# Kernel tuning notes

Hardware: AMD Instinct MI355X
Metric: run time of the kernel (lower is better)

The kernel has to match this reference:

```python
import jax, jax.numpy as jnp
import numpy as np

N, H, W, K = 4, 512, 512, 8
V, F = 50000, 100000
SIGMA, GAMMA = 1e-4, 1e-4
ZNEAR, ZFAR = 1.0, 100.0
EPS = 1e-10


def setup_inputs() -> dict:
    key = jax.random.key(0)
    k1, k2, k3, k4, k5, k6 = jax.random.split(key, 6)
    vn = jax.random.normal(k1, (V, 3), dtype=jnp.float32)
    verts_normals = vn / jnp.linalg.norm(vn, axis=-1, keepdims=True)
    bary = jax.random.uniform(k2, (N, H, W, K, 3), dtype=jnp.float32)
    bary_coords = bary / bary.sum(-1, keepdims=True)  # valid barycentrics
    dists = jax.random.normal(k3, (N, H, W, K), dtype=jnp.float32) * 1e-4
    zbuf = jax.random.uniform(k4, (N, H, W, K), dtype=jnp.float32) * (ZFAR - ZNEAR) + ZNEAR
    faces = jax.random.randint(k5, (F, 3), 0, V, dtype=jnp.int64)
    # include -1 entries (background pixels), as in real rasterizer output
    pix_to_face = jax.random.randint(k6, (N, H, W, K), -1, F, dtype=jnp.int64)
    return {"verts_normals": verts_normals, "bary_coords": bary_coords,
            "dists": dists, "zbuf": zbuf, "faces": faces,
            "pix_to_face": pix_to_face}


def reference(verts_normals, bary_coords, dists, zbuf, faces, pix_to_face):
    # --- normal_shading: gather + barycentric interpolation of vertex normals ---
    faces_normals = verts_normals[faces]                      # (F, 3verts, 3)
    mask = pix_to_face >= 0                                   # (N,H,W,K)
    idx = jnp.where(mask, pix_to_face, 0)
    attrs = faces_normals[idx]                                # (N,H,W,K,3verts,3)
    colors = jnp.einsum('nhwkv,nhwkvc->nhwkc', bary_coords, attrs)
    colors = colors * mask[..., None]                         # zero masked pixels
    opacity = jnp.ones(mask.shape, dtype=colors.dtype)        # torch.ones_like
    # --- softmax_rgb_blend ---
    maskf = mask.astype(colors.dtype)
    prob_map = jax.nn.sigmoid(-dists / SIGMA) * maskf
    alpha = jnp.prod(1.0 - prob_map, axis=-1)                 # (N,H,W)
    z_inv = (ZFAR - zbuf) / (ZFAR - ZNEAR) * maskf
    z_inv_max = jnp.max(z_inv, axis=-1, keepdims=True)
    weights_num = prob_map * jnp.exp((z_inv - z_inv_max) / GAMMA) * opacity
    delta = jnp.maximum(jnp.exp((EPS - z_inv_max) / GAMMA), EPS)
    denom = weights_num.sum(-1, keepdims=True) + delta        # (N,H,W,1)
    background = jnp.array([1.0, 1.0, 1.0], dtype=colors.dtype)
    weighted_colors = jnp.einsum('nhwk,nhwkc->nhwc', weights_num, colors)
    rgb = (weighted_colors + delta * background) / denom      # (N,H,W,3)
    a = (1.0 - alpha)[..., None]                              # (N,H,W,1)
    return jnp.concatenate([rgb, a], axis=-1)                 # (N,H,W,4)
```

## Files before the change

### kernel.cpp

```cpp
#include <hip/hip_runtime.h>
#include <hip/hip_fp16.h>


constexpr int   N_PIX      = 4 * 512 * 512;
constexpr int   N_FRAG     = N_PIX * 8;
constexpr int   N_BLOCKS   = 2048;
constexpr int   N_THREADS  = N_BLOCKS * 256;
constexpr int   N_ITERS    = N_FRAG / N_THREADS;
constexpr float INV_SIGMA  = 1.0f / 1e-4f;
constexpr float INV_GAMMA  = 1.0f / 1e-4f;
constexpr float ZFARV      = 100.0f;
constexpr float INV_ZRANGE = 1.0f / 99.0f;
constexpr float EPSV       = 1e-10f;

__global__ __launch_bounds__(256)
void build_face_normals_kernel(const float* __restrict__ vn,
                               const int*   __restrict__ faces,
                               __half*      __restrict__ fnh,
                               int nf)
{
    int f = blockIdx.x * blockDim.x + threadIdx.x;
    if (f >= nf) return;
    int v0 = faces[3 * f + 0];
    int v1 = faces[3 * f + 1];
    int v2 = faces[3 * f + 2];
    union { ushort us[16]; uint4 u4[2]; } row;
    row.us[0] = __half_as_ushort(__float2half(vn[3 * v0 + 0]));
    row.us[1] = __half_as_ushort(__float2half(vn[3 * v0 + 1]));
    row.us[2] = __half_as_ushort(__float2half(vn[3 * v0 + 2]));
    row.us[3] = __half_as_ushort(__float2half(vn[3 * v1 + 0]));
    row.us[4] = __half_as_ushort(__float2half(vn[3 * v1 + 1]));
    row.us[5] = __half_as_ushort(__float2half(vn[3 * v1 + 2]));
    row.us[6] = __half_as_ushort(__float2half(vn[3 * v2 + 0]));
    row.us[7] = __half_as_ushort(__float2half(vn[3 * v2 + 1]));
    row.us[8] = __half_as_ushort(__float2half(vn[3 * v2 + 2]));
    row.us[9] = 0; row.us[10] = 0; row.us[11] = 0;
    row.us[12] = 0; row.us[13] = 0; row.us[14] = 0; row.us[15] = 0;
    uint4* dst = reinterpret_cast<uint4*>(fnh + 16 * (size_t)f);
    dst[0] = row.u4[0];
    dst[1] = row.u4[1];
}

__global__ __launch_bounds__(256, 8)
void shade_kernel(const float*  __restrict__ bary,
                  const float*  __restrict__ dists,
                  const float*  __restrict__ zbuf,
                  const int*    __restrict__ p2f,
                  const __half* __restrict__ fnh,
                  float*        __restrict__ out)
{
    int gid = blockIdx.x * 256 + threadIdx.x;
    int kk  = threadIdx.x & 7;

    float nd  = dists[gid];
    float nz  = zbuf[gid];
    int   nf_ = p2f[gid];
    size_t nbo = 3 * (size_t)gid;
    float nb0 = bary[nbo + 0];
    float nb1 = bary[nbo + 1];
    float nb2 = bary[nbo + 2];

#pragma unroll
    for (int it = 0; it < N_ITERS; ++it) {
        float d  = nd, zb = nz;
        int   f  = nf_;
        float b0 = nb0, b1 = nb1, b2 = nb2;

        int gn = gid + N_THREADS;
        if (it + 1 < N_ITERS) {
            nd  = dists[gn];
            nz  = zbuf[gn];
            nf_ = p2f[gn];
            size_t bo = 3 * (size_t)gn;
            nb0 = bary[bo + 0];
            nb1 = bary[bo + 1];
            nb2 = bary[bo + 2];
        }

        bool  m  = f >= 0;
        float pr = m ? __builtin_amdgcn_rcpf(1.0f + __expf(d * INV_SIGMA)) : 0.0f;
        float zi = m ? (ZFARV - zb) * INV_ZRANGE : 0.0f;

        float zmax = zi;
        zmax = fmaxf(zmax, __shfl_xor(zmax, 1));
        zmax = fmaxf(zmax, __shfl_xor(zmax, 2));
        zmax = fmaxf(zmax, __shfl_xor(zmax, 4));

        float am = 1.0f - pr;
        am *= __shfl_xor(am, 1);
        am *= __shfl_xor(am, 2);
        am *= __shfl_xor(am, 4);

        float w  = pr * __expf((zi - zmax) * INV_GAMMA);
        int   fe = (w != 0.0f) ? f : 0;

        const __half* hp = fnh + 16 * (size_t)fe;
        uint4 a  = *reinterpret_cast<const uint4*>(hp);
        uint  b8 = reinterpret_cast<const uint*>(hp)[4];
        float2 q0 = __half22float2(*reinterpret_cast<const __half2*>(&a.x));
        float2 q1 = __half22float2(*reinterpret_cast<const __half2*>(&a.y));
        float2 q2 = __half22float2(*reinterpret_cast<const __half2*>(&a.z));
        float2 q3 = __half22float2(*reinterpret_cast<const __half2*>(&a.w));
        float2 q4 = __half22float2(*reinterpret_cast<const __half2*>(&b8));

        float cr = w * (b0 * q0.x + b1 * q1.y + b2 * q3.x);
        float cg = w * (b0 * q0.y + b1 * q2.x + b2 * q3.y);
        float cb = w * (b0 * q1.x + b1 * q2.y + b2 * q4.x);
        float ws = w;

        ws += __shfl_xor(ws, 1);  cr += __shfl_xor(cr, 1);
        cg += __shfl_xor(cg, 1);  cb += __shfl_xor(cb, 1);
        ws += __shfl_xor(ws, 2);  cr += __shfl_xor(cr, 2);
        cg += __shfl_xor(cg, 2);  cb += __shfl_xor(cb, 2);
        ws += __shfl_xor(ws, 4);  cr += __shfl_xor(cr, 4);
        cg += __shfl_xor(cg, 4);  cb += __shfl_xor(cb, 4);

        if (kk == 0) {
            float delta     = fmaxf(__expf((EPSV - zmax) * INV_GAMMA), EPSV);
            float inv_denom = __builtin_amdgcn_rcpf(ws + delta);
            float4 o;
            o.x = (cr + delta) * inv_denom;
            o.y = (cg + delta) * inv_denom;
            o.z = (cb + delta) * inv_denom;
            o.w = 1.0f - am;
            reinterpret_cast<float4*>(out)[gid >> 3] = o;
        }
        gid = gn;
    }
}

extern "C" void kernel_launch(void* const* d_in, const int* in_sizes, int n_in,
                              void* d_out, int out_size, void* d_ws, size_t ws_size,
                              hipStream_t stream) {
    const float* vn    = (const float*)d_in[0];
    const float* bary  = (const float*)d_in[1];
    const float* dists = (const float*)d_in[2];
    const float* zbuf  = (const float*)d_in[3];
    const int*   faces = (const int*)d_in[4];
    const int*   p2f   = (const int*)d_in[5];
    float*       out   = (float*)d_out;

    int nf = in_sizes[4] / 3;
    __half* fnh = (__half*)d_ws;

    build_face_normals_kernel<<<(nf + 255) / 256, 256, 0, stream>>>(vn, faces, fnh, nf);
    shade_kernel<<<N_BLOCKS, 256, 0, stream>>>(bary, dists, zbuf, p2f, fnh, out);
}
```

Before: 232.7 us.

## Split shading into weight pass and sparse gather-resolve pass over surviving fragments

The fused shading kernel becomes two passes. The first reads fragments with float4 vector loads, two threads per pixel, and computes the softmax weights. It compacts the at most two fragments with nonzero weight into a 32-byte per-pixel slot holding face ids and fp16-packed weighted barycentrics. The second pass gathers face normals only for those surviving faces, falling back to a full 8-fragment recompute when more survive. This targets the per-fragment random gathers in the face-normal table, at the cost of an extra kernel launch, a slot buffer write and read, and fp16 rounding of the weighted barycentrics.

```diff
diff --git a/kernel.cpp b/kernel.cpp
--- a/kernel.cpp
+++ b/kernel.cpp
@@ -4,14 +4,23 @@
 
 constexpr int   N_PIX      = 4 * 512 * 512;
 constexpr int   N_FRAG     = N_PIX * 8;
-constexpr int   N_BLOCKS   = 2048;
-constexpr int   N_THREADS  = N_BLOCKS * 256;
-constexpr int   N_ITERS    = N_FRAG / N_THREADS;
 constexpr float INV_SIGMA  = 1.0f / 1e-4f;
 constexpr float INV_GAMMA  = 1.0f / 1e-4f;
 constexpr float ZFARV      = 100.0f;
 constexpr float INV_ZRANGE = 1.0f / 99.0f;
 constexpr float EPSV       = 1e-10f;
+
+__device__ __forceinline__ uint pack_h2(float a, float b) {
+    uint ua = (uint)__half_as_ushort(__float2half_rn(a));
+    uint ub = (uint)__half_as_ushort(__float2half_rn(b));
+    return ua | (ub << 16);
+}
+__device__ __forceinline__ float unp_lo(uint u) {
+    return __half2float(__ushort_as_half((ushort)(u & 0xffffu)));
+}
+__device__ __forceinline__ float unp_hi(uint u) {
+    return __half2float(__ushort_as_half((ushort)(u >> 16)));
+}
 
 __global__ __launch_bounds__(256)
 void build_face_normals_kernel(const float* __restrict__ vn,
@@ -41,91 +50,276 @@
     dst[1] = row.u4[1];
 }
 
-__global__ __launch_bounds__(256, 8)
-void shade_kernel(const float*  __restrict__ bary,
-                  const float*  __restrict__ dists,
-                  const float*  __restrict__ zbuf,
-                  const int*    __restrict__ p2f,
-                  const __half* __restrict__ fnh,
-                  float*        __restrict__ out)
+__global__ __launch_bounds__(256)
+void p1_weights_kernel(const float4* __restrict__ bary4,
+                       const float4* __restrict__ d4p,
+                       const float4* __restrict__ z4p,
+                       const int4*   __restrict__ f4p,
+                       uint4*        __restrict__ slots)
 {
     int gid = blockIdx.x * 256 + threadIdx.x;
-    int kk  = threadIdx.x & 7;
-
-    float nd  = dists[gid];
-    float nz  = zbuf[gid];
-    int   nf_ = p2f[gid];
-    size_t nbo = 3 * (size_t)gid;
-    float nb0 = bary[nbo + 0];
-    float nb1 = bary[nbo + 1];
-    float nb2 = bary[nbo + 2];
-
-#pragma unroll
-    for (int it = 0; it < N_ITERS; ++it) {
-        float d  = nd, zb = nz;
-        int   f  = nf_;
-        float b0 = nb0, b1 = nb1, b2 = nb2;
-
-        int gn = gid + N_THREADS;
-        if (it + 1 < N_ITERS) {
-            nd  = dists[gn];
-            nz  = zbuf[gn];
-            nf_ = p2f[gn];
-            size_t bo = 3 * (size_t)gn;
-            nb0 = bary[bo + 0];
-            nb1 = bary[bo + 1];
-            nb2 = bary[bo + 2];
-        }
-
-        bool  m  = f >= 0;
-        float pr = m ? __builtin_amdgcn_rcpf(1.0f + __expf(d * INV_SIGMA)) : 0.0f;
-        float zi = m ? (ZFARV - zb) * INV_ZRANGE : 0.0f;
-
-        float zmax = zi;
-        zmax = fmaxf(zmax, __shfl_xor(zmax, 1));
-        zmax = fmaxf(zmax, __shfl_xor(zmax, 2));
-        zmax = fmaxf(zmax, __shfl_xor(zmax, 4));
-
-        float am = 1.0f - pr;
-        am *= __shfl_xor(am, 1);
-        am *= __shfl_xor(am, 2);
-        am *= __shfl_xor(am, 4);
-
-        float w  = pr * __expf((zi - zmax) * INV_GAMMA);
-        int   fe = (w != 0.0f) ? f : 0;
-
-        const __half* hp = fnh + 16 * (size_t)fe;
-        uint4 a  = *reinterpret_cast<const uint4*>(hp);
-        uint  b8 = reinterpret_cast<const uint*>(hp)[4];
-        float2 q0 = __half22float2(*reinterpret_cast<const __half2*>(&a.x));
-        float2 q1 = __half22float2(*reinterpret_cast<const __half2*>(&a.y));
-        float2 q2 = __half22float2(*reinterpret_cast<const __half2*>(&a.z));
-        float2 q3 = __half22float2(*reinterpret_cast<const __half2*>(&a.w));
-        float2 q4 = __half22float2(*reinterpret_cast<const __half2*>(&b8));
-
-        float cr = w * (b0 * q0.x + b1 * q1.y + b2 * q3.x);
-        float cg = w * (b0 * q0.y + b1 * q2.x + b2 * q3.y);
-        float cb = w * (b0 * q1.x + b1 * q2.y + b2 * q4.x);
-        float ws = w;
-
-        ws += __shfl_xor(ws, 1);  cr += __shfl_xor(cr, 1);
-        cg += __shfl_xor(cg, 1);  cb += __shfl_xor(cb, 1);
-        ws += __shfl_xor(ws, 2);  cr += __shfl_xor(cr, 2);
-        cg += __shfl_xor(cg, 2);  cb += __shfl_xor(cb, 2);
-        ws += __shfl_xor(ws, 4);  cr += __shfl_xor(cr, 4);
-        cg += __shfl_xor(cg, 4);  cb += __shfl_xor(cb, 4);
-
-        if (kk == 0) {
-            float delta     = fmaxf(__expf((EPSV - zmax) * INV_GAMMA), EPSV);
-            float inv_denom = __builtin_amdgcn_rcpf(ws + delta);
-            float4 o;
-            o.x = (cr + delta) * inv_denom;
-            o.y = (cg + delta) * inv_denom;
-            o.z = (cb + delta) * inv_denom;
-            o.w = 1.0f - am;
-            reinterpret_cast<float4*>(out)[gid >> 3] = o;
-        }
-        gid = gn;
+    int h   = gid & 1;
+
+    float4 d4 = d4p[gid];
+    float4 z4 = z4p[gid];
+    int4   f4 = f4p[gid];
+    const float4* bp = bary4 + 3 * (size_t)gid;
+    float4 b0 = bp[0], b1 = bp[1], b2 = bp[2];
+
+    float dk[4] = {d4.x, d4.y, d4.z, d4.w};
+    float zk[4] = {z4.x, z4.y, z4.z, z4.w};
+    int   fk[4] = {f4.x, f4.y, f4.z, f4.w};
+    float bf[12] = {b0.x, b0.y, b0.z, b0.w, b1.x, b1.y, b1.z, b1.w,
+                    b2.x, b2.y, b2.z, b2.w};
+
+    float pr[4], zi[4];
+#pragma unroll
+    for (int k = 0; k < 4; ++k) {
+        bool m = fk[k] >= 0;
+        pr[k] = m ? __builtin_amdgcn_rcpf(1.0f + __expf(dk[k] * INV_SIGMA)) : 0.0f;
+        zi[k] = m ? (ZFARV - zk[k]) * INV_ZRANGE : 0.0f;
+    }
+
+    float zmax = fmaxf(fmaxf(zi[0], zi[1]), fmaxf(zi[2], zi[3]));
+    zmax = fmaxf(zmax, __shfl_xor(zmax, 1));
+
+    float am = (1.0f - pr[0]) * (1.0f - pr[1]) * (1.0f - pr[2]) * (1.0f - pr[3]);
+    am *= __shfl_xor(am, 1);
+
+    float w[4];
+#pragma unroll
+    for (int k = 0; k < 4; ++k)
+        w[k] = pr[k] * __expf((zi[k] - zmax) * INV_GAMMA);
+
+    float ws = (w[0] + w[1]) + (w[2] + w[3]);
+    ws += __shfl_xor(ws, 1);
+
+    float delta = fmaxf(__expf((EPSV - zmax) * INV_GAMMA), EPSV);
+    float inv   = __builtin_amdgcn_rcpf(ws + delta);
+    float base  = delta * inv;
+
+    int   lf0 = -1, lf1 = -1, lcnt = 0;
+    float c0x = 0.f, c0y = 0.f, c0z = 0.f;
+    float c1x = 0.f, c1y = 0.f, c1z = 0.f;
+#pragma unroll
+    for (int k = 0; k < 4; ++k) {
+        if (w[k] != 0.0f) {
+            float cw = w[k] * inv;
+            if (lcnt == 0) {
+                lf0 = fk[k];
+                c0x = cw * bf[3 * k + 0];
+                c0y = cw * bf[3 * k + 1];
+                c0z = cw * bf[3 * k + 2];
+            } else if (lcnt == 1) {
+                lf1 = fk[k];
+                c1x = cw * bf[3 * k + 0];
+                c1y = cw * bf[3 * k + 1];
+                c1z = cw * bf[3 * k + 2];
+            }
+            ++lcnt;
+        }
+    }
+
+    int   pcnt = __shfl_xor(lcnt, 1);
+    int   pf0  = __shfl_xor(lf0, 1);
+    int   pf1  = __shfl_xor(lf1, 1);
+    float p0x = __shfl_xor(c0x, 1), p0y = __shfl_xor(c0y, 1), p0z = __shfl_xor(c0z, 1);
+    float p1x = __shfl_xor(c1x, 1), p1y = __shfl_xor(c1y, 1), p1z = __shfl_xor(c1z, 1);
+
+    int total = lcnt + pcnt;
+    int   F0, F1;
+    float S0x, S0y, S0z, S1x, S1y, S1z;
+    if (lcnt == 0) {
+        F0 = pf0; S0x = p0x; S0y = p0y; S0z = p0z;
+        F1 = pf1; S1x = p1x; S1y = p1y; S1z = p1z;
+    } else if (lcnt == 1) {
+        F0 = lf0; S0x = c0x; S0y = c0y; S0z = c0z;
+        F1 = pf0; S1x = p0x; S1y = p0y; S1z = p0z;
+    } else {
+        F0 = lf0; S0x = c0x; S0y = c0y; S0z = c0z;
+        F1 = lf1; S1x = c1x; S1y = c1y; S1z = c1z;
+    }
+    if (total > 2) F1 = -2;
+
+    if (h == 0) {
+        int pix = gid >> 1;
+        uint4 q0;
+        q0.x = __float_as_uint(base);
+        q0.y = __float_as_uint(am);
+        q0.z = (uint)F0;
+        q0.w = (uint)F1;
+        uint4 q1;
+        q1.x = pack_h2(S0x, S0y);
+        q1.y = pack_h2(S0z, S1x);
+        q1.z = pack_h2(S1y, S1z);
+        q1.w = 0u;
+        slots[2 * (size_t)pix + 0] = q0;
+        slots[2 * (size_t)pix + 1] = q1;
+    }
+}
+
+__global__ __launch_bounds__(256)
+void p2_resolve_kernel(const uint4*  __restrict__ slots,
+                       const __half* __restrict__ fnh,
+                       const float*  __restrict__ dists,
+                       const float*  __restrict__ zbuf,
+                       const int*    __restrict__ p2f,
+                       const float*  __restrict__ bary,
+                       float4*       __restrict__ out)
+{
+    int pix = blockIdx.x * 256 + threadIdx.x;
+    if (pix >= N_PIX) return;
+
+    uint4 q0 = slots[2 * (size_t)pix + 0];
+    uint4 q1 = slots[2 * (size_t)pix + 1];
+    float base = __uint_as_float(q0.x);
+    float am   = __uint_as_float(q0.y);
+    int   F0   = (int)q0.z;
+    int   F1   = (int)q0.w;
+
+    float r, g, b;
+
+    if (F1 != -2) {
+        r = base; g = base; b = base;
+        if (F0 >= 0) {
+            const __half* hp = fnh + 16 * (size_t)F0;
+            uint4 a  = *reinterpret_cast<const uint4*>(hp);
+            uint  b8 = reinterpret_cast<const uint*>(hp)[4];
+            float2 n01 = __half22float2(*reinterpret_cast<const __half2*>(&a.x));
+            float2 n23 = __half22float2(*reinterpret_cast<const __half2*>(&a.y));
+            float2 n45 = __half22float2(*reinterpret_cast<const __half2*>(&a.z));
+            float2 n67 = __half22float2(*reinterpret_cast<const __half2*>(&a.w));
+            float2 n8x = __half22float2(*reinterpret_cast<const __half2*>(&b8));
+            float cb0 = unp_lo(q1.x), cb1 = unp_hi(q1.x), cb2 = unp_lo(q1.y);
+            r += cb0 * n01.x + cb1 * n23.y + cb2 * n67.x;
+            g += cb0 * n01.y + cb1 * n45.x + cb2 * n67.y;
+            b += cb0 * n23.x + cb1 * n45.y + cb2 * n8x.x;
+        }
+        if (F1 >= 0) {
+            const __half* hp = fnh + 16 * (size_t)F1;
+            uint4 a  = *reinterpret_cast<const uint4*>(hp);
+            uint  b8 = reinterpret_cast<const uint*>(hp)[4];
+            float2 n01 = __half22float2(*reinterpret_cast<const __half2*>(&a.x));
+            float2 n23 = __half22float2(*reinterpret_cast<const __half2*>(&a.y));
+            float2 n45 = __half22float2(*reinterpret_cast<const __half2*>(&a.z));
+            float2 n67 = __half22float2(*reinterpret_cast<const __half2*>(&a.w));
+            float2 n8x = __half22float2(*reinterpret_cast<const __half2*>(&b8));
+            float cb0 = unp_hi(q1.y), cb1 = unp_lo(q1.z), cb2 = unp_hi(q1.z);
+            r += cb0 * n01.x + cb1 * n23.y + cb2 * n67.x;
+            g += cb0 * n01.y + cb1 * n45.x + cb2 * n67.y;
+            b += cb0 * n23.x + cb1 * n45.y + cb2 * n8x.x;
+        }
+    } else {
+        float pr8[8], zi8[8], w8[8];
+        int   ff8[8];
+        float zmax = 0.0f;
+        am = 1.0f;
+#pragma unroll
+        for (int k = 0; k < 8; ++k) {
+            float d  = dists[8 * (size_t)pix + k];
+            float zb = zbuf[8 * (size_t)pix + k];
+            int   f  = p2f[8 * (size_t)pix + k];
+            ff8[k] = f;
+            bool m = f >= 0;
+            pr8[k] = m ? __builtin_amdgcn_rcpf(1.0f + __expf(d * INV_SIGMA)) : 0.0f;
+            zi8[k] = m ? (ZFARV - zb) * INV_ZRANGE : 0.0f;
+            zmax   = fmaxf(zmax, zi8[k]);
+            am    *= (1.0f - pr8[k]);
+        }
+        float ws = 0.0f;
+#pragma unroll
+        for (int k = 0; k < 8; ++k) {
+            w8[k] = pr8[k] * __expf((zi8[k] - zmax) * INV_GAMMA);
+            ws += w8[k];
+        }
+        float delta = fmaxf(__expf((EPSV - zmax) * INV_GAMMA), EPSV);
+        float inv   = __builtin_amdgcn_rcpf(ws + delta);
+        base = delta * inv;
+        r = base; g = base; b = base;
+#pragma unroll
+        for (int k = 0; k < 8; ++k) {
+            if (w8[k] != 0.0f) {
+                float cw = w8[k] * inv;
+                float bb0 = bary[24 * (size_t)pix + 3 * k + 0];
+                float bb1 = bary[24 * (size_t)pix + 3 * k + 1];
+                float bb2 = bary[24 * (size_t)pix + 3 * k + 2];
+                const __half* hp = fnh + 16 * (size_t)ff8[k];
+                uint4 a  = *reinterpret_cast<const uint4*>(hp);
+                uint  b8v = reinterpret_cast<const uint*>(hp)[4];
+                float2 n01 = __half22float2(*reinterpret_cast<const __half2*>(&a.x));
+                float2 n23 = __half22float2(*reinterpret_cast<const __half2*>(&a.y));
+                float2 n45 = __half22float2(*reinterpret_cast<const __half2*>(&a.z));
+                float2 n67 = __half22float2(*reinterpret_cast<const __half2*>(&a.w));
+                float2 n8x = __half22float2(*reinterpret_cast<const __half2*>(&b8v));
+                r += cw * (bb0 * n01.x + bb1 * n23.y + bb2 * n67.x);
+                g += cw * (bb0 * n01.y + bb1 * n45.x + bb2 * n67.y);
+                b += cw * (bb0 * n23.x + bb1 * n45.y + bb2 * n8x.x);
+            }
+        }
+    }
+
+    float4 o;
+    o.x = r; o.y = g; o.z = b; o.w = 1.0f - am;
+    out[pix] = o;
+}
+
+__global__ __launch_bounds__(256)
+void shade_fallback_kernel(const float*  __restrict__ bary,
+                           const float*  __restrict__ dists,
+                           const float*  __restrict__ zbuf,
+                           const int*    __restrict__ p2f,
+                           const __half* __restrict__ fnh,
+                           float*        __restrict__ out)
+{
+    int gid = blockIdx.x * 256 + threadIdx.x;
+    if (gid >= N_FRAG) return;
+    int kk = gid & 7;
+    float d  = dists[gid];
+    float zb = zbuf[gid];
+    int   f  = p2f[gid];
+    float b0 = bary[3 * (size_t)gid + 0];
+    float b1 = bary[3 * (size_t)gid + 1];
+    float b2 = bary[3 * (size_t)gid + 2];
+    bool  m  = f >= 0;
+    float pr = m ? __builtin_amdgcn_rcpf(1.0f + __expf(d * INV_SIGMA)) : 0.0f;
+    float zi = m ? (ZFARV - zb) * INV_ZRANGE : 0.0f;
+    float zmax = zi;
+    zmax = fmaxf(zmax, __shfl_xor(zmax, 1));
+    zmax = fmaxf(zmax, __shfl_xor(zmax, 2));
+    zmax = fmaxf(zmax, __shfl_xor(zmax, 4));
+    float am = 1.0f - pr;
+    am *= __shfl_xor(am, 1);
+    am *= __shfl_xor(am, 2);
+    am *= __shfl_xor(am, 4);
+    float w  = pr * __expf((zi - zmax) * INV_GAMMA);
+    int   fe = (w != 0.0f) ? f : 0;
+    const __half* hp = fnh + 16 * (size_t)fe;
+    uint4 a  = *reinterpret_cast<const uint4*>(hp);
+    uint  b8 = reinterpret_cast<const uint*>(hp)[4];
+    float2 n01 = __half22float2(*reinterpret_cast<const __half2*>(&a.x));
+    float2 n23 = __half22float2(*reinterpret_cast<const __half2*>(&a.y));
+    float2 n45 = __half22float2(*reinterpret_cast<const __half2*>(&a.z));
+    float2 n67 = __half22float2(*reinterpret_cast<const __half2*>(&a.w));
+    float2 n8x = __half22float2(*reinterpret_cast<const __half2*>(&b8));
+    float cr = w * (b0 * n01.x + b1 * n23.y + b2 * n67.x);
+    float cg = w * (b0 * n01.y + b1 * n45.x + b2 * n67.y);
+    float cb = w * (b0 * n23.x + b1 * n45.y + b2 * n8x.x);
+    float ws = w;
+    ws += __shfl_xor(ws, 1);  cr += __shfl_xor(cr, 1);
+    cg += __shfl_xor(cg, 1);  cb += __shfl_xor(cb, 1);
+    ws += __shfl_xor(ws, 2);  cr += __shfl_xor(cr, 2);
+    cg += __shfl_xor(cg, 2);  cb += __shfl_xor(cb, 2);
+    ws += __shfl_xor(ws, 4);  cr += __shfl_xor(cr, 4);
+    cg += __shfl_xor(cg, 4);  cb += __shfl_xor(cb, 4);
+    if (kk == 0) {
+        float delta     = fmaxf(__expf((EPSV - zmax) * INV_GAMMA), EPSV);
+        float inv_denom = __builtin_amdgcn_rcpf(ws + delta);
+        float4 o;
+        o.x = (cr + delta) * inv_denom;
+        o.y = (cg + delta) * inv_denom;
+        o.z = (cb + delta) * inv_denom;
+        o.w = 1.0f - am;
+        reinterpret_cast<float4*>(out)[gid >> 3] = o;
     }
 }
 
@@ -141,8 +335,26 @@
     float*       out   = (float*)d_out;
 
     int nf = in_sizes[4] / 3;
+
+    size_t table_bytes = (size_t)nf * 32;
+    size_t slot_bytes  = (size_t)N_PIX * 32;
     __half* fnh = (__half*)d_ws;
 
     build_face_normals_kernel<<<(nf + 255) / 256, 256, 0, stream>>>(vn, faces, fnh, nf);
-    shade_kernel<<<N_BLOCKS, 256, 0, stream>>>(bary, dists, zbuf, p2f, fnh, out);
-}
+
+    if (ws_size >= table_bytes + slot_bytes) {
+        uint4* slots = (uint4*)((char*)d_ws + table_bytes);
+        p1_weights_kernel<<<(N_PIX * 2) / 256, 256, 0, stream>>>(
+            reinterpret_cast<const float4*>(bary),
+            reinterpret_cast<const float4*>(dists),
+            reinterpret_cast<const float4*>(zbuf),
+            reinterpret_cast<const int4*>(p2f),
+            slots);
+        p2_resolve_kernel<<<N_PIX / 256, 256, 0, stream>>>(
+            slots, fnh, dists, zbuf, p2f, bary,
+            reinterpret_cast<float4*>(out));
+    } else {
+        shade_fallback_kernel<<<N_FRAG / 256, 256, 0, stream>>>(
+            bary, dists, zbuf, p2f, fnh, out);
+    }
+}
```

Result: slower. 249.4 us (+7.2%).

## Use one fragment per thread and skip bary/normal loads for zero-weight fragments

Applied to the files above, without the earlier changes.

Drops the persistent grid-stride loop with software prefetching and launches one thread per fragment instead. The barycentric and face-normal loads now sit inside a branch that runs only when the blend weight is nonzero, so the many fragments whose weight underflows to zero (because of the steep softmax) never fetch that memory. The cost is losing the explicit prefetch overlap and launching many more blocks, and the branch may still fetch whole cache lines of bary when any lane in the wave needs them.

```diff
diff --git a/kernel.cpp b/kernel.cpp
--- a/kernel.cpp
+++ b/kernel.cpp
@@ -4,9 +4,6 @@
 
 constexpr int   N_PIX      = 4 * 512 * 512;
 constexpr int   N_FRAG     = N_PIX * 8;
-constexpr int   N_BLOCKS   = 2048;
-constexpr int   N_THREADS  = N_BLOCKS * 256;
-constexpr int   N_ITERS    = N_FRAG / N_THREADS;
 constexpr float INV_SIGMA  = 1.0f / 1e-4f;
 constexpr float INV_GAMMA  = 1.0f / 1e-4f;
 constexpr float ZFARV      = 100.0f;
@@ -52,80 +49,61 @@
     int gid = blockIdx.x * 256 + threadIdx.x;
     int kk  = threadIdx.x & 7;
 
-    float nd  = dists[gid];
-    float nz  = zbuf[gid];
-    int   nf_ = p2f[gid];
-    size_t nbo = 3 * (size_t)gid;
-    float nb0 = bary[nbo + 0];
-    float nb1 = bary[nbo + 1];
-    float nb2 = bary[nbo + 2];
+    float d  = dists[gid];
+    float zb = zbuf[gid];
+    int   f  = p2f[gid];
 
-#pragma unroll
-    for (int it = 0; it < N_ITERS; ++it) {
-        float d  = nd, zb = nz;
-        int   f  = nf_;
-        float b0 = nb0, b1 = nb1, b2 = nb2;
+    bool  m  = f >= 0;
+    float pr = m ? __builtin_amdgcn_rcpf(1.0f + __expf(d * INV_SIGMA)) : 0.0f;
+    float zi = m ? (ZFARV - zb) * INV_ZRANGE : 0.0f;
 
-        int gn = gid + N_THREADS;
-        if (it + 1 < N_ITERS) {
-            nd  = dists[gn];
-            nz  = zbuf[gn];
-            nf_ = p2f[gn];
-            size_t bo = 3 * (size_t)gn;
-            nb0 = bary[bo + 0];
-            nb1 = bary[bo + 1];
-            nb2 = bary[bo + 2];
-        }
+    float zmax = zi;
+    zmax = fmaxf(zmax, __shfl_xor(zmax, 1));
+    zmax = fmaxf(zmax, __shfl_xor(zmax, 2));
+    zmax = fmaxf(zmax, __shfl_xor(zmax, 4));
 
-        bool  m  = f >= 0;
-        float pr = m ? __builtin_amdgcn_rcpf(1.0f + __expf(d * INV_SIGMA)) : 0.0f;
-        float zi = m ? (ZFARV - zb) * INV_ZRANGE : 0.0f;
+    float am = 1.0f - pr;
+    am *= __shfl_xor(am, 1);
+    am *= __shfl_xor(am, 2);
+    am *= __shfl_xor(am, 4);
 
-        float zmax = zi;
-        zmax = fmaxf(zmax, __shfl_xor(zmax, 1));
-        zmax = fmaxf(zmax, __shfl_xor(zmax, 2));
-        zmax = fmaxf(zmax, __shfl_xor(zmax, 4));
+    float w = pr * __expf((zi - zmax) * INV_GAMMA);
 
-        float am = 1.0f - pr;
-        am *= __shfl_xor(am, 1);
-        am *= __shfl_xor(am, 2);
-        am *= __shfl_xor(am, 4);
+    float cr = 0.0f, cg = 0.0f, cb = 0.0f;
+    if (w != 0.0f) {
+        float b0 = bary[3 * (size_t)gid + 0];
+        float b1 = bary[3 * (size_t)gid + 1];
+        float b2 = bary[3 * (size_t)gid + 2];
+        const __half* hp = fnh + 16 * (size_t)f;
+        uint4 a  = *reinterpret_cast<const uint4*>(hp);
+        uint  u8 = reinterpret_cast<const uint*>(hp)[4];
+        float2 n01 = __half22float2(*reinterpret_cast<const __half2*>(&a.x));
+        float2 n23 = __half22float2(*reinterpret_cast<const __half2*>(&a.y));
+        float2 n45 = __half22float2(*reinterpret_cast<const __half2*>(&a.z));
+        float2 n67 = __half22float2(*reinterpret_cast<const __half2*>(&a.w));
+        float2 n8x = __half22float2(*reinterpret_cast<const __half2*>(&u8));
+        cr = w * (b0 * n01.x + b1 * n23.y + b2 * n67.x);
+        cg = w * (b0 * n01.y + b1 * n45.x + b2 * n67.y);
+        cb = w * (b0 * n23.x + b1 * n45.y + b2 * n8x.x);
+    }
 
-        float w  = pr * __expf((zi - zmax) * INV_GAMMA);
-        int   fe = (w != 0.0f) ? f : 0;
+    float ws = w;
+    ws += __shfl_xor(ws, 1);  cr += __shfl_xor(cr, 1);
+    cg += __shfl_xor(cg, 1);  cb += __shfl_xor(cb, 1);
+    ws += __shfl_xor(ws, 2);  cr += __shfl_xor(cr, 2);
+    cg += __shfl_xor(cg, 2);  cb += __shfl_xor(cb, 2);
+    ws += __shfl_xor(ws, 4);  cr += __shfl_xor(cr, 4);
+    cg += __shfl_xor(cg, 4);  cb += __shfl_xor(cb, 4);
 
-        const __half* hp = fnh + 16 * (size_t)fe;
-        uint4 a  = *reinterpret_cast<const uint4*>(hp);
-        uint  b8 = reinterpret_cast<const uint*>(hp)[4];
-        float2 q0 = __half22float2(*reinterpret_cast<const __half2*>(&a.x));
-        float2 q1 = __half22float2(*reinterpret_cast<const __half2*>(&a.y));
-        float2 q2 = __half22float2(*reinterpret_cast<const __half2*>(&a.z));
-        float2 q3 = __half22float2(*reinterpret_cast<const __half2*>(&a.w));
-        float2 q4 = __half22float2(*reinterpret_cast<const __half2*>(&b8));
-
-        float cr = w * (b0 * q0.x + b1 * q1.y + b2 * q3.x);
-        float cg = w * (b0 * q0.y + b1 * q2.x + b2 * q3.y);
-        float cb = w * (b0 * q1.x + b1 * q2.y + b2 * q4.x);
-        float ws = w;
-
-        ws += __shfl_xor(ws, 1);  cr += __shfl_xor(cr, 1);
-        cg += __shfl_xor(cg, 1);  cb += __shfl_xor(cb, 1);
-        ws += __shfl_xor(ws, 2);  cr += __shfl_xor(cr, 2);
-        cg += __shfl_xor(cg, 2);  cb += __shfl_xor(cb, 2);
-        ws += __shfl_xor(ws, 4);  cr += __shfl_xor(cr, 4);
-        cg += __shfl_xor(cg, 4);  cb += __shfl_xor(cb, 4);
-
-        if (kk == 0) {
-            float delta     = fmaxf(__expf((EPSV - zmax) * INV_GAMMA), EPSV);
-            float inv_denom = __builtin_amdgcn_rcpf(ws + delta);
-            float4 o;
-            o.x = (cr + delta) * inv_denom;
-            o.y = (cg + delta) * inv_denom;
-            o.z = (cb + delta) * inv_denom;
-            o.w = 1.0f - am;
-            reinterpret_cast<float4*>(out)[gid >> 3] = o;
-        }
-        gid = gn;
+    if (kk == 0) {
+        float delta     = fmaxf(__expf((EPSV - zmax) * INV_GAMMA), EPSV);
+        float inv_denom = __builtin_amdgcn_rcpf(ws + delta);
+        float4 o;
+        o.x = (cr + delta) * inv_denom;
+        o.y = (cg + delta) * inv_denom;
+        o.z = (cb + delta) * inv_denom;
+        o.w = 1.0f - am;
+        reinterpret_cast<float4*>(out)[gid >> 3] = o;
     }
 }
 
@@ -144,5 +122,5 @@
     __half* fnh = (__half*)d_ws;
 
     build_face_normals_kernel<<<(nf + 255) / 256, 256, 0, stream>>>(vn, faces, fnh, nf);
-    shade_kernel<<<N_BLOCKS, 256, 0, stream>>>(bary, dists, zbuf, p2f, fnh, out);
+    shade_kernel<<<N_FRAG / 256, 256, 0, stream>>>(bary, dists, zbuf, p2f, fnh, out);
 }
```

New measurement: 227.0 us. 2.5% less time.
